# Kernel optimization log

Measured on AMD Instinct MI355X. Metric: run time of the kernel, lower is better.

Reference implementation:

```python
import jax, jax.numpy as jnp
import numpy as np

D = 256; NH = 8; NL = 4; NP = 4; DFF = 2048; HD = D // NH
SHAPES = [(64, 64), (32, 32), (16, 16), (8, 8)]
B = 2; LEN = sum(h * w for h, w in SHAPES)


def setup_inputs() -> dict:
    key = jax.random.key(0)
    ks = jax.random.split(key, 12)
    def w(k, shape, s=0.02):
        return jax.random.normal(k, shape, jnp.float32) * s
    starts = np.cumsum([0] + [h * w for h, w in SHAPES[:-1]])
    return {
        "src": jax.random.normal(ks[0], (B, LEN, D), jnp.float32),
        "pos": jax.random.normal(ks[1], (B, LEN, D), jnp.float32) * 0.1,
        "spatial_shapes": jnp.array(SHAPES, dtype=jnp.int32),
        "level_start_index": jnp.array(starts, dtype=jnp.int32),
        "w_value": w(ks[2], (D, D)), "b_value": jnp.zeros((D,), jnp.float32),
        "w_off": w(ks[3], (D, NH * NL * NP * 2)), "b_off": w(ks[4], (NH * NL * NP * 2,), 0.1),
        "w_attn": w(ks[5], (D, NH * NL * NP)), "b_attn": jnp.zeros((NH * NL * NP,), jnp.float32),
        "w_out": w(ks[6], (D, D)), "b_out": jnp.zeros((D,), jnp.float32),
        "w1": w(ks[7], (D, DFF)), "b1": jnp.zeros((DFF,), jnp.float32),
        "w2": w(ks[8], (DFF, D)), "b2": jnp.zeros((D,), jnp.float32),
        "g1": jnp.ones((D,), jnp.float32), "be1": jnp.zeros((D,), jnp.float32),
        "g2": jnp.ones((D,), jnp.float32), "be2": jnp.zeros((D,), jnp.float32),
    }


def _layer_norm(x, g, b):
    mu = jnp.mean(x, -1, keepdims=True)
    v = jnp.var(x, -1, keepdims=True)
    return (x - mu) * jax.lax.rsqrt(v + 1e-5) * g + b


def _reference_points(shapes):
    # torch.linspace(0.5, H-0.5, H)/H == (arange(H)+0.5)/H
    refs = []
    for H, W in shapes:
        ry = (jnp.arange(H, dtype=jnp.float32) + 0.5) / H
        rx = (jnp.arange(W, dtype=jnp.float32) + 0.5) / W
        yy, xx = jnp.meshgrid(ry, rx, indexing='ij')
        refs.append(jnp.stack([xx.ravel(), yy.ravel()], -1))
    return jnp.concatenate(refs, 0)  # (Len, 2) as (x, y)


def _ms_deform_sample(value, loc, shapes):
    # value: (B, Len, NH, HD); loc: (B, Lq, NH, NL, NP, 2) normalized [0,1]
    # Replicates torch grid_sample(bilinear, padding='zeros', align_corners=False).
    Bn, Lq = loc.shape[0], loc.shape[1]
    P = loc.shape[4]
    start = 0
    outs = []
    for lvl, (H, W) in enumerate(shapes):
        v = value[:, start:start + H * W].transpose(0, 2, 1, 3)  # (B, NH, HW, HD)
        start += H * W
        l = loc[:, :, :, lvl]                      # (B, Lq, NH, P, 2)
        x = l[..., 0] * W - 0.5
        y = l[..., 1] * H - 0.5
        x0 = jnp.floor(x); y0 = jnp.floor(y)
        dx = x - x0; dy = y - y0
        x0i = x0.astype(jnp.int32); y0i = y0.astype(jnp.int32)
        acc = None
        for xi, yi, wgt in ((x0i, y0i, (1 - dx) * (1 - dy)),
                            (x0i + 1, y0i, dx * (1 - dy)),
                            (x0i, y0i + 1, (1 - dx) * dy),
                            (x0i + 1, y0i + 1, dx * dy)):
            valid = ((xi >= 0) & (xi < W) & (yi >= 0) & (yi < H)).astype(value.dtype)
            idx = jnp.clip(yi, 0, H - 1) * W + jnp.clip(xi, 0, W - 1)  # (B, Lq, NH, P)
            idx = idx.transpose(0, 2, 1, 3).reshape(Bn, NH, Lq * P)
            g = jnp.take_along_axis(v, idx[..., None], axis=2).reshape(Bn, NH, Lq, P, HD)
            w = (wgt * valid).transpose(0, 2, 1, 3)[..., None]  # (B, NH, Lq, P, 1)
            acc = g * w if acc is None else acc + g * w
        outs.append(acc)  # (B, NH, Lq, P, HD)
    return jnp.stack(outs, 3)  # (B, NH, Lq, NL, NP, HD)


def _forward(src, pos, w_value, b_value, w_off, b_off, w_attn, b_attn,
             w_out, b_out, w1, b1, w2, b2, g1, be1, g2, be2, shapes):
    Bn, Lq, _ = src.shape
    q = src + pos  # with_pos_embed
    value = (src @ w_value + b_value).reshape(Bn, Lq, NH, HD)
    off = (q @ w_off + b_off).reshape(Bn, Lq, NH, NL, NP, 2)
    attn = jax.nn.softmax((q @ w_attn + b_attn).reshape(Bn, Lq, NH, NL * NP), -1)
    attn = attn.reshape(Bn, Lq, NH, NL, NP)
    ref = _reference_points(shapes)  # (Len, 2)
    normalizer = jnp.array([[w_, h_] for h_, w_ in shapes], jnp.float32)  # (NL, 2) = (W, H)
    loc = ref[None, :, None, None, None, :] + off / normalizer[None, None, None, :, None, :]
    sampled = _ms_deform_sample(value, loc, shapes)  # (B, NH, Lq, NL, NP, HD)
    out = jnp.einsum('bqhlp,bhqlpd->bqhd', attn, sampled).reshape(Bn, Lq, D)
    out = out @ w_out + b_out
    x = _layer_norm(src + out, g1, be1)           # residual + norm1
    ff = jax.nn.relu(x @ w1 + b1) @ w2 + b2       # FFN (dropout=0)
    return _layer_norm(x + ff, g2, be2)           # residual + norm2


def reference(src, pos, spatial_shapes, level_start_index, w_value, b_value,
              w_off, b_off, w_attn, b_attn, w_out, b_out, w1, b1, w2, b2,
              g1, be1, g2, be2):
    shapes = [tuple(int(v) for v in s) for s in np.asarray(spatial_shapes)]
    return _forward(src, pos, w_value, b_value, w_off, b_off, w_attn, b_attn,
                    w_out, b_out, w1, b1, w2, b2, g1, be1, g2, be2, shapes)
```

## Files before the change

### kernel.cpp

```cpp
#include <hip/hip_runtime.h>
#include <math.h>

#define D 256
#define NH 8
#define NL 4
#define NP 4
#define DFF 2048
#define HD 32
#define BB 2
#define LEN 5440
#define MROWS (BB * LEN)

typedef __attribute__((ext_vector_type(8))) short short8;
typedef __attribute__((ext_vector_type(4))) float f32x4;
typedef unsigned int uint32;

__device__ __forceinline__ unsigned short f2bf(float f) {
    uint32 u = __float_as_uint(f);
    u += 0x7FFF + ((u >> 16) & 1);
    return (unsigned short)(u >> 16);
}
__device__ __forceinline__ float bf2f(unsigned short h) {
    return __uint_as_float(((uint32)h) << 16);
}
__device__ __forceinline__ uint32 pack2(float a, float b) {
    return (uint32)f2bf(a) | ((uint32)f2bf(b) << 16);
}

__device__ __forceinline__ void swz85(int b, int ncols, int& row, int& col) {
    const int gsz = ncols << 3;
    const int full = 10 * gsz;
    if (b < full) {
        const int g = b / gsz, idx = b - g * gsz;
        row = (g << 3) + (idx & 7);
        col = idx >> 3;
    } else {
        const int idx = b - full;
        row = 80 + idx % 5;
        col = idx / 5;
    }
}

__global__ void prep(const float* __restrict__ w_value, const float* __restrict__ w_off,
                     const float* __restrict__ w_attn, const float* __restrict__ w_out,
                     const float* __restrict__ w1, const float* __restrict__ w2,
                     const float* __restrict__ b_value, const float* __restrict__ b_off,
                     const float* __restrict__ b_attn,
                     unsigned short* __restrict__ wqvT, unsigned short* __restrict__ woT,
                     unsigned short* __restrict__ w1T, unsigned short* __restrict__ w2T,
                     float* __restrict__ bqv) {
    const int blk = blockIdx.x;
    if (blk >= 1248) {
        for (int i = threadIdx.x; i < 640; i += 256)
            bqv[i] = (i < 256) ? b_value[i] : (i < 512 ? b_off[i - 256] : b_attn[i - 512]);
        return;
    }
    const float* W; unsigned short* WT; int K, N, tid;
    if (blk < 64)       { W = w_value; WT = wqvT;             K = 256;  N = 256;  tid = blk; }
    else if (blk < 128) { W = w_off;   WT = wqvT + 256 * 256; K = 256;  N = 256;  tid = blk - 64; }
    else if (blk < 160) { W = w_attn;  WT = wqvT + 512 * 256; K = 256;  N = 128;  tid = blk - 128; }
    else if (blk < 224) { W = w_out;   WT = woT;              K = 256;  N = 256;  tid = blk - 160; }
    else if (blk < 736) { W = w1;      WT = w1T;              K = 256;  N = 2048; tid = blk - 224; }
    else                { W = w2;      WT = w2T;              K = 2048; N = 256;  tid = blk - 736; }
    const int ntx = N >> 5;
    const int nb = (tid % ntx) * 32, kb = (tid / ntx) * 32;

    __shared__ float tile[32][33];
    const int tx = threadIdx.x & 31, ty = threadIdx.x >> 5;
#pragma unroll
    for (int i = 0; i < 32; i += 8)
        tile[ty + i][tx] = W[(size_t)(kb + ty + i) * N + nb + tx];
    __syncthreads();
#pragma unroll
    for (int i = 0; i < 32; i += 8)
        WT[(size_t)(nb + ty + i) * K + kb + tx] = f2bf(tile[tx][ty + i]);
}

__global__ __launch_bounds__(256) void ffn1_gemm(
        const unsigned short* __restrict__ A,
        const unsigned short* __restrict__ BT, const float* __restrict__ bias,
        unsigned short* __restrict__ Cv, int N, int K, int lda, int ldb) {
    __shared__ unsigned short Ash[128][40];
    __shared__ unsigned short Bsh[128][40];

    int rowt, colt;
    swz85(blockIdx.x, N >> 7, rowt, colt);
    const int row0 = rowt * 128, col0 = colt * 128;

    const int t = threadIdx.x;
    const int wave = t >> 6, lane = t & 63;
    const int wr = wave >> 1, wc = wave & 1;
    const int lrow = lane & 15, quad = lane >> 4;
    const int srow = t >> 1;
    const int cb = (t & 1) * 16;

    const unsigned short* ap = A + (size_t)(row0 + srow) * lda + cb;
    const unsigned short* bp = BT + (size_t)(col0 + srow) * ldb + cb;

    f32x4 acc[4][4];
#pragma unroll
    for (int i = 0; i < 4; i++)
#pragma unroll
        for (int j = 0; j < 4; j++) acc[i][j] = (f32x4){0.f, 0.f, 0.f, 0.f};

    uint4 ra0 = *(const uint4*)(ap + 0), ra1 = *(const uint4*)(ap + 8);
    uint4 rb0 = *(const uint4*)(bp + 0), rb1 = *(const uint4*)(bp + 8);

    for (int kb = 0; kb < K; kb += 32) {
        __syncthreads();
        *(uint4*)&Ash[srow][cb + 0] = ra0;
        *(uint4*)&Ash[srow][cb + 8] = ra1;
        *(uint4*)&Bsh[srow][cb + 0] = rb0;
        *(uint4*)&Bsh[srow][cb + 8] = rb1;
        __syncthreads();
        if (kb + 32 < K) {
            ra0 = *(const uint4*)(ap + kb + 32 + 0);
            ra1 = *(const uint4*)(ap + kb + 32 + 8);
            rb0 = *(const uint4*)(bp + kb + 32 + 0);
            rb1 = *(const uint4*)(bp + kb + 32 + 8);
        }

        short8 af[4], bfr[4];
#pragma unroll
        for (int mt = 0; mt < 4; mt++)
            af[mt] = *(const short8*)&Ash[wr * 64 + mt * 16 + lrow][quad * 8];
#pragma unroll
        for (int nt = 0; nt < 4; nt++)
            bfr[nt] = *(const short8*)&Bsh[wc * 64 + nt * 16 + lrow][quad * 8];
#pragma unroll
        for (int mt = 0; mt < 4; mt++)
#pragma unroll
            for (int nt = 0; nt < 4; nt++)
                acc[mt][nt] = __builtin_amdgcn_mfma_f32_16x16x32_bf16(
                    af[mt], bfr[nt], acc[mt][nt], 0, 0, 0);
    }

#pragma unroll
    for (int nt = 0; nt < 4; nt++) {
        const int col = col0 + wc * 64 + nt * 16 + lrow;
        const float bv = bias[col];
#pragma unroll
        for (int mt = 0; mt < 4; mt++) {
            f32x4 a = acc[mt][nt];
#pragma unroll
            for (int r = 0; r < 4; r++) {
                const int row = row0 + wr * 64 + mt * 16 + quad * 4 + r;
                Cv[(size_t)row * N + col] = f2bf(fmaxf(a[r] + bv, 0.f));
            }
        }
    }
}

template <int NZ>
__global__ __launch_bounds__(256) void splitk_gemm(
        const unsigned short* __restrict__ A, const unsigned short* __restrict__ BT,
        float* __restrict__ part, int KC, int lda, int ldb) {
    __shared__ unsigned short Ash[128][40];
    __shared__ unsigned short Bsh[128][40];

    int rowt, cc;
    swz85(blockIdx.x, 2 * NZ, rowt, cc);
    const int row0 = rowt * 128;
    const int col0 = (cc & 1) * 128;
    const int z = cc >> 1;
    const int koff = z * KC;
    float* __restrict__ C = part + (size_t)z * MROWS * 256;

    const int t = threadIdx.x;
    const int wave = t >> 6, lane = t & 63;
    const int wr = wave >> 1, wc = wave & 1;
    const int lrow = lane & 15, quad = lane >> 4;
    const int srow = t >> 1;
    const int cb = (t & 1) * 16;

    const unsigned short* ap = A + (size_t)(row0 + srow) * lda + koff + cb;
    const unsigned short* bp = BT + (size_t)(col0 + srow) * ldb + koff + cb;

    f32x4 acc[4][4];
#pragma unroll
    for (int i = 0; i < 4; i++)
#pragma unroll
        for (int j = 0; j < 4; j++) acc[i][j] = (f32x4){0.f, 0.f, 0.f, 0.f};

    uint4 ra0 = *(const uint4*)(ap + 0), ra1 = *(const uint4*)(ap + 8);
    uint4 rb0 = *(const uint4*)(bp + 0), rb1 = *(const uint4*)(bp + 8);

    for (int kb = 0; kb < KC; kb += 32) {
        __syncthreads();
        *(uint4*)&Ash[srow][cb + 0] = ra0;
        *(uint4*)&Ash[srow][cb + 8] = ra1;
        *(uint4*)&Bsh[srow][cb + 0] = rb0;
        *(uint4*)&Bsh[srow][cb + 8] = rb1;
        __syncthreads();
        if (kb + 32 < KC) {
            ra0 = *(const uint4*)(ap + kb + 32 + 0);
            ra1 = *(const uint4*)(ap + kb + 32 + 8);
            rb0 = *(const uint4*)(bp + kb + 32 + 0);
            rb1 = *(const uint4*)(bp + kb + 32 + 8);
        }

        short8 af[4], bfr[4];
#pragma unroll
        for (int mt = 0; mt < 4; mt++)
            af[mt] = *(const short8*)&Ash[wr * 64 + mt * 16 + lrow][quad * 8];
#pragma unroll
        for (int nt = 0; nt < 4; nt++)
            bfr[nt] = *(const short8*)&Bsh[wc * 64 + nt * 16 + lrow][quad * 8];
#pragma unroll
        for (int mt = 0; mt < 4; mt++)
#pragma unroll
            for (int nt = 0; nt < 4; nt++)
                acc[mt][nt] = __builtin_amdgcn_mfma_f32_16x16x32_bf16(
                    af[mt], bfr[nt], acc[mt][nt], 0, 0, 0);
    }

#pragma unroll
    for (int nt = 0; nt < 4; nt++) {
        const int col = col0 + wc * 64 + nt * 16 + lrow;
#pragma unroll
        for (int mt = 0; mt < 4; mt++) {
            f32x4 a = acc[mt][nt];
#pragma unroll
            for (int r = 0; r < 4; r++) {
                const int row = row0 + wr * 64 + mt * 16 + quad * 4 + r;
                C[(size_t)row * 256 + col] = a[r];
            }
        }
    }
}

__global__ __launch_bounds__(256) void qv_gemm(
        const float* __restrict__ src, const float* __restrict__ pos,
        const unsigned short* __restrict__ BT, const float* __restrict__ bias,
        unsigned short* __restrict__ val, float* __restrict__ qout) {
    __shared__ unsigned short Ash[128][40];
    __shared__ unsigned short Bsh[128][40];

    int rowt, colt;
    swz85(blockIdx.x, 5, rowt, colt);
    const int row0 = rowt * 128, col0 = colt * 128;
    const bool addp = (col0 >= 256);

    const int t = threadIdx.x;
    const int wave = t >> 6, lane = t & 63;
    const int wr = wave >> 1, wc = wave & 1;
    const int lrow = lane & 15, quad = lane >> 4;
    const int srow = t >> 1;
    const int cb = (t & 1) * 16;

    const float* ap = src + (size_t)(row0 + srow) * 256 + cb;
    const float* pp = pos + (size_t)(row0 + srow) * 256 + cb;
    const unsigned short* bp = BT + (size_t)(col0 + srow) * 256 + cb;

    f32x4 acc[4][4];
#pragma unroll
    for (int i = 0; i < 4; i++)
#pragma unroll
        for (int j = 0; j < 4; j++) acc[i][j] = (f32x4){0.f, 0.f, 0.f, 0.f};

    float4 fa[4]; float4 fp[4]; uint4 rb0, rb1;
#pragma unroll
    for (int j = 0; j < 4; j++) fa[j] = *(const float4*)(ap + 4 * j);
    if (addp) {
#pragma unroll
        for (int j = 0; j < 4; j++) fp[j] = *(const float4*)(pp + 4 * j);
    }
    rb0 = *(const uint4*)(bp + 0);
    rb1 = *(const uint4*)(bp + 8);

    for (int kb = 0; kb < 256; kb += 32) {
        __syncthreads();
        {
            float4 f0 = fa[0], f1 = fa[1], f2 = fa[2], f3 = fa[3];
            if (addp) {
                f0.x += fp[0].x; f0.y += fp[0].y; f0.z += fp[0].z; f0.w += fp[0].w;
                f1.x += fp[1].x; f1.y += fp[1].y; f1.z += fp[1].z; f1.w += fp[1].w;
                f2.x += fp[2].x; f2.y += fp[2].y; f2.z += fp[2].z; f2.w += fp[2].w;
                f3.x += fp[3].x; f3.y += fp[3].y; f3.z += fp[3].z; f3.w += fp[3].w;
            }
            uint4 u0 = make_uint4(pack2(f0.x, f0.y), pack2(f0.z, f0.w),
                                  pack2(f1.x, f1.y), pack2(f1.z, f1.w));
            uint4 u1 = make_uint4(pack2(f2.x, f2.y), pack2(f2.z, f2.w),
                                  pack2(f3.x, f3.y), pack2(f3.z, f3.w));
            *(uint4*)&Ash[srow][cb + 0] = u0;
            *(uint4*)&Ash[srow][cb + 8] = u1;
            *(uint4*)&Bsh[srow][cb + 0] = rb0;
            *(uint4*)&Bsh[srow][cb + 8] = rb1;
        }
        __syncthreads();
        if (kb + 32 < 256) {
#pragma unroll
            for (int j = 0; j < 4; j++) fa[j] = *(const float4*)(ap + kb + 32 + 4 * j);
            if (addp) {
#pragma unroll
                for (int j = 0; j < 4; j++) fp[j] = *(const float4*)(pp + kb + 32 + 4 * j);
            }
            rb0 = *(const uint4*)(bp + kb + 32 + 0);
            rb1 = *(const uint4*)(bp + kb + 32 + 8);
        }

        short8 af[4], bfr[4];
#pragma unroll
        for (int mt = 0; mt < 4; mt++)
            af[mt] = *(const short8*)&Ash[wr * 64 + mt * 16 + lrow][quad * 8];
#pragma unroll
        for (int nt = 0; nt < 4; nt++)
            bfr[nt] = *(const short8*)&Bsh[wc * 64 + nt * 16 + lrow][quad * 8];
#pragma unroll
        for (int mt = 0; mt < 4; mt++)
#pragma unroll
            for (int nt = 0; nt < 4; nt++)
                acc[mt][nt] = __builtin_amdgcn_mfma_f32_16x16x32_bf16(
                    af[mt], bfr[nt], acc[mt][nt], 0, 0, 0);
    }

#pragma unroll
    for (int nt = 0; nt < 4; nt++) {
        const int col = col0 + wc * 64 + nt * 16 + lrow;
        const float bv = bias[col];
#pragma unroll
        for (int mt = 0; mt < 4; mt++) {
            f32x4 a = acc[mt][nt];
#pragma unroll
            for (int r = 0; r < 4; r++) {
                const int row = row0 + wr * 64 + mt * 16 + quad * 4 + r;
                float v = a[r] + bv;
                if (col < 256)
                    val[(size_t)row * 256 + col] = f2bf(v);
                else
                    qout[(size_t)row * 384 + (col - 256)] = v;
            }
        }
    }
}

__global__ void sampler(const unsigned short* __restrict__ val, const float* __restrict__ qout,
                        unsigned short* __restrict__ out) {
    __shared__ __align__(16) int   sIdx[128][4];
    __shared__ __align__(16) float sW[128][4];
    const int bq = blockIdx.x;
    const int b = bq / LEN, q = bq % LEN;
    const int t = threadIdx.x;

    if (t < 128) {
        const int h = t >> 4, p = t & 15;
        const int l = p >> 2;

        float refx, refy;
        if (q < 4096) {
            int rq = q >> 6, cq = q & 63;
            refx = (cq + 0.5f) * (1.0f / 64.0f);
            refy = (rq + 0.5f) * (1.0f / 64.0f);
        } else if (q < 5120) {
            int qq = q - 4096;
            int rq = qq >> 5, cq = qq & 31;
            refx = (cq + 0.5f) * (1.0f / 32.0f);
            refy = (rq + 0.5f) * (1.0f / 32.0f);
        } else if (q < 5376) {
            int qq = q - 5120;
            int rq = qq >> 4, cq = qq & 15;
            refx = (cq + 0.5f) * (1.0f / 16.0f);
            refy = (rq + 0.5f) * (1.0f / 16.0f);
        } else {
            int qq = q - 5376;
            int rq = qq >> 3, cq = qq & 7;
            refx = (cq + 0.5f) * (1.0f / 8.0f);
            refy = (rq + 0.5f) * (1.0f / 8.0f);
        }

        float lv = qout[(size_t)bq * 384 + 256 + t];
        float mx = lv;
#pragma unroll
        for (int o = 1; o < 16; o <<= 1) mx = fmaxf(mx, __shfl_xor(mx, o, 16));
        float e = expf(lv - mx);
        float s = e;
#pragma unroll
        for (int o = 1; o < 16; o <<= 1) s += __shfl_xor(s, o, 16);
        const float aw = e / s;

        const float ox = qout[(size_t)bq * 384 + h * 32 + p * 2 + 0];
        const float oy = qout[(size_t)bq * 384 + h * 32 + p * 2 + 1];

        const int LST[4] = {0, 4096, 5120, 5376};
        const int WW = 64 >> l;
        const float rw = 1.0f / (float)WW;

        float x = (refx + ox * rw) * (float)WW - 0.5f;
        float y = (refy + oy * rw) * (float)WW - 0.5f;
        float x0f = floorf(x), y0f = floorf(y);
        float dx = x - x0f, dy = y - y0f;
        int x0 = (int)x0f, y0 = (int)y0f;

        const int base = (b * LEN + LST[l]) * 256 + h * 32;
        int4 iv; float4 wv;
        {
            int xs[2] = {x0, x0 + 1}, ys[2] = {y0, y0 + 1};
            float wx[2] = {1.f - dx, dx}, wy[2] = {1.f - dy, dy};
            int ic[4]; float wc4[4];
#pragma unroll
            for (int cy = 0; cy < 2; cy++)
#pragma unroll
                for (int cx = 0; cx < 2; cx++) {
                    int xi = xs[cx], yi = ys[cy];
                    bool vld = (xi >= 0) && (xi < WW) && (yi >= 0) && (yi < WW);
                    int xc = min(max(xi, 0), WW - 1);
                    int yc = min(max(yi, 0), WW - 1);
                    ic[cy * 2 + cx] = base + (yc * WW + xc) * 256;
                    wc4[cy * 2 + cx] = vld ? wx[cx] * wy[cy] * aw : 0.f;
                }
            iv = make_int4(ic[0], ic[1], ic[2], ic[3]);
            wv = make_float4(wc4[0], wc4[1], wc4[2], wc4[3]);
        }
        *(int4*)&sIdx[t][0] = iv;
        *(float4*)&sW[t][0] = wv;
    }
    __syncthreads();

    const int h = t >> 5, d = t & 31;
    const unsigned short* vald = val + d;
    float acc = 0.f;
#pragma unroll 4
    for (int p = 0; p < 16; p++) {
        const int r = h * 16 + p;
        int4 iv = *(const int4*)&sIdx[r][0];
        float4 wv = *(const float4*)&sW[r][0];
        acc += bf2f(vald[iv.x]) * wv.x;
        acc += bf2f(vald[iv.y]) * wv.y;
        acc += bf2f(vald[iv.z]) * wv.z;
        acc += bf2f(vald[iv.w]) * wv.w;
    }
    out[(size_t)bq * D + h * HD + d] = f2bf(acc);
}

template <int NPART>
__global__ void add_lnN(const float* __restrict__ part, const float* __restrict__ bias,
                        const float* __restrict__ rsd,
                        const float* __restrict__ g, const float* __restrict__ be,
                        float* __restrict__ out, unsigned short* __restrict__ out16) {
    __shared__ float r1[4], r2[4];
    const int row = blockIdx.x, t = threadIdx.x;
    const size_t i = (size_t)row * D + t;
    float v = bias[t] + rsd[i];
#pragma unroll
    for (int z = 0; z < NPART; z++) v += part[(size_t)z * MROWS * 256 + i];
    float s1 = v, s2 = v * v;
#pragma unroll
    for (int o = 32; o > 0; o >>= 1) {
        s1 += __shfl_down(s1, o, 64);
        s2 += __shfl_down(s2, o, 64);
    }
    if ((t & 63) == 0) { r1[t >> 6] = s1; r2[t >> 6] = s2; }
    __syncthreads();
    float su = r1[0] + r1[1] + r1[2] + r1[3];
    float sq = r2[0] + r2[1] + r2[2] + r2[3];
    float mean = su * (1.0f / D);
    float var = fmaxf(sq * (1.0f / D) - mean * mean, 0.f);
    const float o = (v - mean) * rsqrtf(var + 1e-5f) * g[t] + be[t];
    out[i] = o;
    if (out16) out16[i] = f2bf(o);
}

extern "C" void kernel_launch(void* const* d_in, const int* in_sizes, int n_in,
                              void* d_out, int out_size, void* d_ws, size_t ws_size,
                              hipStream_t stream) {
    const float* src     = (const float*)d_in[0];
    const float* pos     = (const float*)d_in[1];
    const float* w_value = (const float*)d_in[4];
    const float* b_value = (const float*)d_in[5];
    const float* w_off   = (const float*)d_in[6];
    const float* b_off   = (const float*)d_in[7];
    const float* w_attn  = (const float*)d_in[8];
    const float* b_attn  = (const float*)d_in[9];
    const float* w_out   = (const float*)d_in[10];
    const float* b_out   = (const float*)d_in[11];
    const float* w1      = (const float*)d_in[12];
    const float* b1      = (const float*)d_in[13];
    const float* w2      = (const float*)d_in[14];
    const float* b2      = (const float*)d_in[15];
    const float* g1      = (const float*)d_in[16];
    const float* be1     = (const float*)d_in[17];
    const float* g2      = (const float*)d_in[18];
    const float* be2     = (const float*)d_in[19];
    float* out = (float*)d_out;

    size_t off = 0;
    auto alloc = [&](size_t bytes) -> char* {
        char* p = (char*)d_ws + off;
        off += (bytes + 255) & ~(size_t)255;
        return p;
    };
    unsigned short* wqvT = (unsigned short*)alloc((size_t)640 * 256 * 2);
    unsigned short* woT  = (unsigned short*)alloc(256 * 256 * 2);
    unsigned short* w1T  = (unsigned short*)alloc((size_t)2048 * 256 * 2);
    unsigned short* w2T  = (unsigned short*)alloc((size_t)256 * 2048 * 2);
    float* bqv           = (float*)alloc(640 * 4);

    float* qout          = (float*)alloc((size_t)MROWS * 384 * 4);
    unsigned short* val  = (unsigned short*)alloc((size_t)MROWS * 256 * 2);
    unsigned short* attn = (unsigned short*)alloc((size_t)MROWS * 256 * 2);
    unsigned short* hb   = (unsigned short*)alloc((size_t)MROWS * 2048 * 2);
    float* xbuf          = (float*)alloc((size_t)MROWS * 256 * 4);
    unsigned short* xb16 = (unsigned short*)alloc((size_t)MROWS * 256 * 2);
    float* part          = (float*)alloc((size_t)4 * MROWS * 256 * 4);

    prep<<<1249, 256, 0, stream>>>(w_value, w_off, w_attn, w_out, w1, w2,
                                   b_value, b_off, b_attn, wqvT, woT, w1T, w2T, bqv);

    qv_gemm<<<425, 256, 0, stream>>>(src, pos, wqvT, bqv, val, qout);
    sampler<<<MROWS, 256, 0, stream>>>(val, qout, attn);
    splitk_gemm<2><<<340, 256, 0, stream>>>(attn, woT, part, 128, 256, 256);
    add_lnN<2><<<MROWS, 256, 0, stream>>>(part, b_out, src, g1, be1, xbuf, xb16);

    ffn1_gemm<<<1360, 256, 0, stream>>>(xb16, w1T, b1, hb, 2048, 256, 256, 256);
    splitk_gemm<4><<<680, 256, 0, stream>>>(hb, w2T, part, 512, 2048, 2048);
    add_lnN<4><<<MROWS, 256, 0, stream>>>(part, b2, xbuf, g2, be2, out, nullptr);
}
```

Baseline: 225.9 us.

## Fuse FFN up and down projections into one kernel keeping hidden in LDS

Replaces the separate FFN1 GEMM (writing a bf16 hidden buffer of MROWS x 2048) and the split-K FFN2 GEMM with one kernel. Each block takes 64 rows and half the hidden dimension, computes relu(x@w1+b1) chunk by chunk into shared memory, and accumulates the w2 product directly. It writes 2-way split-K partials. This removes the large hidden-activation round trip through global memory and one launch. In exchange there are only 340 blocks with a 64-row tile, so occupancy and weight reuse per block are lower and there are many more barriers per block.

```diff
diff --git a/kernel.cpp b/kernel.cpp
--- a/kernel.cpp
+++ b/kernel.cpp
@@ -27,18 +27,23 @@
     return (uint32)f2bf(a) | ((uint32)f2bf(b) << 16);
 }
 
-__device__ __forceinline__ void swz85(int b, int ncols, int& row, int& col) {
+__device__ __forceinline__ void swzg(int b, int nrows, int ncols, int& row, int& col) {
     const int gsz = ncols << 3;
-    const int full = 10 * gsz;
+    const int ngrp = nrows >> 3;
+    const int full = ngrp * gsz;
     if (b < full) {
         const int g = b / gsz, idx = b - g * gsz;
         row = (g << 3) + (idx & 7);
         col = idx >> 3;
     } else {
+        const int rem = nrows - (ngrp << 3);
         const int idx = b - full;
-        row = 80 + idx % 5;
-        col = idx / 5;
-    }
+        row = (ngrp << 3) + idx % rem;
+        col = idx / rem;
+    }
+}
+__device__ __forceinline__ void swz85(int b, int ncols, int& row, int& col) {
+    swzg(b, 85, ncols, row, col);
 }
 
 __global__ void prep(const float* __restrict__ w_value, const float* __restrict__ w_off,
@@ -76,26 +81,32 @@
         WT[(size_t)(nb + ty + i) * K + kb + tx] = f2bf(tile[tx][ty + i]);
 }
 
-__global__ __launch_bounds__(256) void ffn1_gemm(
-        const unsigned short* __restrict__ A,
-        const unsigned short* __restrict__ BT, const float* __restrict__ bias,
-        unsigned short* __restrict__ Cv, int N, int K, int lda, int ldb) {
-    __shared__ unsigned short Ash[128][40];
-    __shared__ unsigned short Bsh[128][40];
-
-    int rowt, colt;
-    swz85(blockIdx.x, N >> 7, rowt, colt);
-    const int row0 = rowt * 128, col0 = colt * 128;
+__global__ __launch_bounds__(256) void ffn_fused(
+        const unsigned short* __restrict__ X,
+        const unsigned short* __restrict__ w1T,
+        const float* __restrict__ b1,
+        const unsigned short* __restrict__ w2T,
+        float* __restrict__ part) {
+    __shared__ unsigned short xsh[64][264];
+    __shared__ unsigned short hsh[64][136];
+    __shared__ unsigned short wsh[256][40];
+
+    int rt, z;
+    swzg(blockIdx.x, 170, 2, rt, z);
+    const int row0 = rt * 64;
+    const int hid0 = z * 1024;
 
     const int t = threadIdx.x;
     const int wave = t >> 6, lane = t & 63;
-    const int wr = wave >> 1, wc = wave & 1;
     const int lrow = lane & 15, quad = lane >> 4;
-    const int srow = t >> 1;
-    const int cb = (t & 1) * 16;
-
-    const unsigned short* ap = A + (size_t)(row0 + srow) * lda + cb;
-    const unsigned short* bp = BT + (size_t)(col0 + srow) * ldb + cb;
+
+    {
+        const int xr = t >> 2, xc = (t & 3) * 64;
+        const unsigned short* xp = X + (size_t)(row0 + xr) * 256 + xc;
+#pragma unroll
+        for (int j = 0; j < 8; j++)
+            *(uint4*)&xsh[xr][xc + j * 8] = *(const uint4*)(xp + j * 8);
+    }
 
     f32x4 acc[4][4];
 #pragma unroll
@@ -103,49 +114,102 @@
 #pragma unroll
         for (int j = 0; j < 4; j++) acc[i][j] = (f32x4){0.f, 0.f, 0.f, 0.f};
 
-    uint4 ra0 = *(const uint4*)(ap + 0), ra1 = *(const uint4*)(ap + 8);
-    uint4 rb0 = *(const uint4*)(bp + 0), rb1 = *(const uint4*)(bp + 8);
-
-    for (int kb = 0; kb < K; kb += 32) {
+    const int s1r = t >> 1, s1c = (t & 1) * 16;
+    const unsigned short* w2base = w2T + (size_t)t * 2048 + hid0;
+
+    for (int c = 0; c < 8; c++) {
+        const int hidc = hid0 + c * 128;
+
+        f32x4 acc1[4][2];
+#pragma unroll
+        for (int i = 0; i < 4; i++)
+#pragma unroll
+            for (int j = 0; j < 2; j++) acc1[i][j] = (f32x4){0.f, 0.f, 0.f, 0.f};
+
+        const unsigned short* w1p = w1T + (size_t)(hidc + s1r) * 256 + s1c;
+        uint4 ra0 = *(const uint4*)(w1p + 0);
+        uint4 ra1 = *(const uint4*)(w1p + 8);
+
+        for (int kb = 0; kb < 256; kb += 32) {
+            __syncthreads();
+            *(uint4*)&wsh[s1r][s1c + 0] = ra0;
+            *(uint4*)&wsh[s1r][s1c + 8] = ra1;
+            __syncthreads();
+            if (kb + 32 < 256) {
+                ra0 = *(const uint4*)(w1p + kb + 32 + 0);
+                ra1 = *(const uint4*)(w1p + kb + 32 + 8);
+            }
+            short8 af[4], bf[2];
+#pragma unroll
+            for (int mt = 0; mt < 4; mt++)
+                af[mt] = *(const short8*)&xsh[mt * 16 + lrow][kb + quad * 8];
+#pragma unroll
+            for (int nt = 0; nt < 2; nt++)
+                bf[nt] = *(const short8*)&wsh[wave * 32 + nt * 16 + lrow][quad * 8];
+#pragma unroll
+            for (int mt = 0; mt < 4; mt++)
+#pragma unroll
+                for (int nt = 0; nt < 2; nt++)
+                    acc1[mt][nt] = __builtin_amdgcn_mfma_f32_16x16x32_bf16(
+                        af[mt], bf[nt], acc1[mt][nt], 0, 0, 0);
+        }
+
+#pragma unroll
+        for (int nt = 0; nt < 2; nt++) {
+            const int hcol = wave * 32 + nt * 16 + lrow;
+            const float bv = b1[hidc + hcol];
+#pragma unroll
+            for (int mt = 0; mt < 4; mt++) {
+                f32x4 a = acc1[mt][nt];
+#pragma unroll
+                for (int r = 0; r < 4; r++)
+                    hsh[mt * 16 + quad * 4 + r][hcol] = f2bf(fmaxf(a[r] + bv, 0.f));
+            }
+        }
         __syncthreads();
-        *(uint4*)&Ash[srow][cb + 0] = ra0;
-        *(uint4*)&Ash[srow][cb + 8] = ra1;
-        *(uint4*)&Bsh[srow][cb + 0] = rb0;
-        *(uint4*)&Bsh[srow][cb + 8] = rb1;
+
+        uint4 rb[4];
+#pragma unroll
+        for (int j = 0; j < 4; j++) rb[j] = *(const uint4*)(w2base + c * 128 + j * 8);
+
+        for (int kb2 = 0; kb2 < 128; kb2 += 32) {
+            __syncthreads();
+#pragma unroll
+            for (int j = 0; j < 4; j++) *(uint4*)&wsh[t][j * 8] = rb[j];
+            __syncthreads();
+            if (kb2 + 32 < 128) {
+#pragma unroll
+                for (int j = 0; j < 4; j++)
+                    rb[j] = *(const uint4*)(w2base + c * 128 + kb2 + 32 + j * 8);
+            }
+            short8 af[4], bf[4];
+#pragma unroll
+            for (int mt = 0; mt < 4; mt++)
+                af[mt] = *(const short8*)&hsh[mt * 16 + lrow][kb2 + quad * 8];
+#pragma unroll
+            for (int nt = 0; nt < 4; nt++)
+                bf[nt] = *(const short8*)&wsh[wave * 64 + nt * 16 + lrow][quad * 8];
+#pragma unroll
+            for (int mt = 0; mt < 4; mt++)
+#pragma unroll
+                for (int nt = 0; nt < 4; nt++)
+                    acc[mt][nt] = __builtin_amdgcn_mfma_f32_16x16x32_bf16(
+                        af[mt], bf[nt], acc[mt][nt], 0, 0, 0);
+        }
         __syncthreads();
-        if (kb + 32 < K) {
-            ra0 = *(const uint4*)(ap + kb + 32 + 0);
-            ra1 = *(const uint4*)(ap + kb + 32 + 8);
-            rb0 = *(const uint4*)(bp + kb + 32 + 0);
-            rb1 = *(const uint4*)(bp + kb + 32 + 8);
-        }
-
-        short8 af[4], bfr[4];
-#pragma unroll
-        for (int mt = 0; mt < 4; mt++)
-            af[mt] = *(const short8*)&Ash[wr * 64 + mt * 16 + lrow][quad * 8];
-#pragma unroll
-        for (int nt = 0; nt < 4; nt++)
-            bfr[nt] = *(const short8*)&Bsh[wc * 64 + nt * 16 + lrow][quad * 8];
-#pragma unroll
-        for (int mt = 0; mt < 4; mt++)
-#pragma unroll
-            for (int nt = 0; nt < 4; nt++)
-                acc[mt][nt] = __builtin_amdgcn_mfma_f32_16x16x32_bf16(
-                    af[mt], bfr[nt], acc[mt][nt], 0, 0, 0);
-    }
-
+    }
+
+    float* C = part + (size_t)z * MROWS * 256;
 #pragma unroll
     for (int nt = 0; nt < 4; nt++) {
-        const int col = col0 + wc * 64 + nt * 16 + lrow;
-        const float bv = bias[col];
+        const int col = wave * 64 + nt * 16 + lrow;
 #pragma unroll
         for (int mt = 0; mt < 4; mt++) {
             f32x4 a = acc[mt][nt];
 #pragma unroll
             for (int r = 0; r < 4; r++) {
-                const int row = row0 + wr * 64 + mt * 16 + quad * 4 + r;
-                Cv[(size_t)row * N + col] = f2bf(fmaxf(a[r] + bv, 0.f));
+                const int row = row0 + mt * 16 + quad * 4 + r;
+                C[(size_t)row * 256 + col] = a[r];
             }
         }
     }
@@ -498,10 +562,9 @@
     float* qout          = (float*)alloc((size_t)MROWS * 384 * 4);
     unsigned short* val  = (unsigned short*)alloc((size_t)MROWS * 256 * 2);
     unsigned short* attn = (unsigned short*)alloc((size_t)MROWS * 256 * 2);
-    unsigned short* hb   = (unsigned short*)alloc((size_t)MROWS * 2048 * 2);
     float* xbuf          = (float*)alloc((size_t)MROWS * 256 * 4);
     unsigned short* xb16 = (unsigned short*)alloc((size_t)MROWS * 256 * 2);
-    float* part          = (float*)alloc((size_t)4 * MROWS * 256 * 4);
+    float* part          = (float*)alloc((size_t)2 * MROWS * 256 * 4);
 
     prep<<<1249, 256, 0, stream>>>(w_value, w_off, w_attn, w_out, w1, w2,
                                    b_value, b_off, b_attn, wqvT, woT, w1T, w2T, bqv);
@@ -511,7 +574,6 @@
     splitk_gemm<2><<<340, 256, 0, stream>>>(attn, woT, part, 128, 256, 256);
     add_lnN<2><<<MROWS, 256, 0, stream>>>(part, b_out, src, g1, be1, xbuf, xb16);
 
-    ffn1_gemm<<<1360, 256, 0, stream>>>(xb16, w1T, b1, hb, 2048, 256, 256, 256);
-    splitk_gemm<4><<<680, 256, 0, stream>>>(hb, w2T, part, 512, 2048, 2048);
-    add_lnN<4><<<MROWS, 256, 0, stream>>>(part, b2, xbuf, g2, be2, out, nullptr);
-}
+    ffn_fused<<<340, 256, 0, stream>>>(xb16, w1T, b1, w2T, part);
+    add_lnN<2><<<MROWS, 256, 0, stream>>>(part, b2, xbuf, g2, be2, out, nullptr);
+}
```

New measurement: 300.3 us. 1.33x slower.
